# Kernel optimization log

Measured on AMD Instinct MI355X. Metric: run time of the kernel, lower is better.

The kernel has to match this reference:

```python
import jax, jax.numpy as jnp
import numpy as np

N_DIM = 256
N_HEAD = 8
HEAD_DIM = N_DIM // N_HEAD  # 32


def setup_inputs() -> dict:
    key = jax.random.key(0)
    k_x, k_wqkv, k_bqkv, k_wp, k_bp = jax.random.split(key, 5)
    B, T, C = 32, 512, N_DIM
    x = jax.random.normal(k_x, (B, T, C), dtype=jnp.float32)
    # nn.Linear default init ~ U(-1/sqrt(fan_in), 1/sqrt(fan_in)); use scaled normal for simplicity
    s = 1.0 / np.sqrt(C)
    W_qkv = jax.random.normal(k_wqkv, (C, 3 * C), dtype=jnp.float32) * s
    b_qkv = jax.random.normal(k_bqkv, (3 * C,), dtype=jnp.float32) * s
    W_proj = jax.random.normal(k_wp, (C, C), dtype=jnp.float32) * s
    b_proj = jax.random.normal(k_bp, (C,), dtype=jnp.float32) * s
    return {"x": x, "W_qkv": W_qkv, "b_qkv": b_qkv, "W_proj": W_proj, "b_proj": b_proj}


def reference(x, W_qkv, b_qkv, W_proj, b_proj):
    B, T, C = x.shape
    H, D = N_HEAD, HEAD_DIM
    qkv = jnp.einsum('btc,cf->btf', x, W_qkv) + b_qkv  # [B,T,3C]
    q, k, v = jnp.split(qkv, 3, axis=2)
    # [B,T,C] -> [B,H,T,D]
    q = q.reshape(B, T, H, D).transpose(0, 2, 1, 3)
    k = k.reshape(B, T, H, D).transpose(0, 2, 1, 3)
    v = v.reshape(B, T, H, D).transpose(0, 2, 1, 3)
    scale = 1.0 / jnp.sqrt(jnp.float32(D))
    scores = jnp.einsum('bhqd,bhkd->bhqk', q, k) * scale  # [B,H,T,T]
    causal = jnp.tril(jnp.ones((T, T), dtype=bool))
    scores = jnp.where(causal, scores, jnp.finfo(scores.dtype).min)
    attn = jax.nn.softmax(scores, axis=-1)
    out = jnp.einsum('bhqk,bhkd->bhqd', attn, v)  # [B,H,T,D]
    out = out.transpose(0, 2, 1, 3).reshape(B, T, C)
    return jnp.einsum('btc,cf->btf', out, W_proj) + b_proj
```

## Files before the change

kernel.cpp:

```cpp
#include <hip/hip_runtime.h>
#include <stdint.h>
#include <stddef.h>

#define NB 32
#define NT 512
#define NC 256
#define NH 8
#define ND 32
#define NQTOT (NB*NH*NT*ND)

typedef __attribute__((ext_vector_type(8))) short short8;
typedef __attribute__((ext_vector_type(4))) float f32x4;

__device__ __forceinline__ unsigned short f2bf(float f) {
    union { float f; unsigned u; } x; x.f = f;
    unsigned r = (x.u + 0x7FFFu + ((x.u >> 16) & 1u)) >> 16;
    return (unsigned short)r;
}

__global__ __launch_bounds__(256) void k_cvt_w2(const float* __restrict__ wqkv,
                                                unsigned short* __restrict__ wqkvT,
                                                const float* __restrict__ wproj,
                                                unsigned short* __restrict__ wprojT) {
    __shared__ float tile[32][33];
    int bid = blockIdx.x;
    const float* w; unsigned short* wt; int N, bx, by;
    if (bid < 192) { w = wqkv; wt = wqkvT; N = 768; bx = bid % 24; by = bid / 24; }
    else { bid -= 192; w = wproj; wt = wprojT; N = 256; bx = bid % 8; by = bid / 8; }
    const int K = 256;
    const int tx = threadIdx.x & 31;
    const int ty = threadIdx.x >> 5;
    const int n0 = bx * 32, k0 = by * 32;
#pragma unroll
    for (int dy = 0; dy < 4; ++dy)
        tile[ty + dy * 8][tx] = w[(size_t)(k0 + ty + dy * 8) * N + n0 + tx];
    __syncthreads();
#pragma unroll
    for (int dy = 0; dy < 4; ++dy)
        wt[(size_t)(n0 + ty + dy * 8) * K + k0 + tx] = f2bf(tile[tx][ty + dy * 8]);
}

template <int EPI>
__global__ __launch_bounds__(256) void k_gemm(const void* __restrict__ Av,
                                              const unsigned short* __restrict__ Bt,
                                              const float* __restrict__ bias,
                                              unsigned short* __restrict__ qkv,
                                              float* __restrict__ outf,
                                              int M, int N, int K) {
    __shared__ unsigned short Al[2][128][40];
    __shared__ unsigned short Bl[2][128][40];

    const int tid = threadIdx.x;
    const int lane = tid & 63;
    const int w = tid >> 6;
    const int wm = w >> 1, wn = w & 1;
    const int i16 = lane & 15, g = lane >> 4;

    const int nbm = M >> 7;
    const int bm = blockIdx.x % nbm;
    const int bn = blockIdx.x / nbm;
    const int m0 = bm << 7, n0 = bn << 7;

    const float* Af = (const float*)Av;
    const unsigned short* Ab = (const unsigned short*)Av;

    f32x4 acc[4][4];
    const f32x4 z4 = {0.f, 0.f, 0.f, 0.f};
#pragma unroll
    for (int a = 0; a < 4; a++)
#pragma unroll
        for (int b = 0; b < 4; b++) acc[a][b] = z4;

    const int row0 = tid >> 2;
    const int cr = tid & 3;

    float4 fa[2][2];
    short8 sa[2];
    short8 sb[2];

    auto LOAD = [&](int k0) {
#pragma unroll
        for (int h = 0; h < 2; ++h) {
            const int row = row0 + h * 64;
            if (EPI == 0) {
                const float* p = &Af[(size_t)(m0 + row) * K + k0 + cr * 8];
                fa[h][0] = *reinterpret_cast<const float4*>(p);
                fa[h][1] = *reinterpret_cast<const float4*>(p + 4);
            } else {
                sa[h] = *reinterpret_cast<const short8*>(&Ab[(size_t)(m0 + row) * K + k0 + cr * 8]);
            }
            sb[h] = *reinterpret_cast<const short8*>(&Bt[(size_t)(n0 + row) * K + k0 + cr * 8]);
        }
    };
    auto STORE = [&](int buf) {
#pragma unroll
        for (int h = 0; h < 2; ++h) {
            const int row = row0 + h * 64;
            if (EPI == 0) {
                short8 t;
                t[0] = (short)f2bf(fa[h][0].x); t[1] = (short)f2bf(fa[h][0].y);
                t[2] = (short)f2bf(fa[h][0].z); t[3] = (short)f2bf(fa[h][0].w);
                t[4] = (short)f2bf(fa[h][1].x); t[5] = (short)f2bf(fa[h][1].y);
                t[6] = (short)f2bf(fa[h][1].z); t[7] = (short)f2bf(fa[h][1].w);
                *reinterpret_cast<short8*>(&Al[buf][row][cr * 8]) = t;
            } else {
                *reinterpret_cast<short8*>(&Al[buf][row][cr * 8]) = sa[h];
            }
            *reinterpret_cast<short8*>(&Bl[buf][row][cr * 8]) = sb[h];
        }
    };

    LOAD(0);
    STORE(0);
    __syncthreads();

    const int nk = K >> 5;
    for (int it = 0; it < nk; ++it) {
        const int cur = it & 1;
        if (it + 1 < nk) LOAD((it + 1) << 5);

        short8 af[4], bf[4];
#pragma unroll
        for (int mi = 0; mi < 4; mi++)
            af[mi] = *reinterpret_cast<const short8*>(&Al[cur][wm * 64 + mi * 16 + i16][g * 8]);
#pragma unroll
        for (int ni = 0; ni < 4; ni++)
            bf[ni] = *reinterpret_cast<const short8*>(&Bl[cur][wn * 64 + ni * 16 + i16][g * 8]);
#pragma unroll
        for (int mi = 0; mi < 4; mi++)
#pragma unroll
            for (int ni = 0; ni < 4; ni++)
                acc[mi][ni] = __builtin_amdgcn_mfma_f32_16x16x32_bf16(af[mi], bf[ni], acc[mi][ni], 0, 0, 0);

        if (it + 1 < nk) STORE(cur ^ 1);
        __syncthreads();
    }

#pragma unroll
    for (int mi = 0; mi < 4; mi++) {
#pragma unroll
        for (int ni = 0; ni < 4; ni++) {
            const int col = n0 + wn * 64 + ni * 16 + i16;
            const float bv = bias[col];
#pragma unroll
            for (int r = 0; r < 4; r++) {
                const int rowg = m0 + wm * 64 + mi * 16 + g * 4 + r;
                const float v = acc[mi][ni][r] + bv;
                if (EPI == 0) {
                    const int which = col >> 8;
                    const int cc = col & 255;
                    const int h = cc >> 5, d = cc & 31;
                    const int bb = rowg >> 9, t = rowg & 511;
                    qkv[(size_t)which * NQTOT +
                        ((((size_t)bb * NH + h) * NT + t) * ND) + d] = f2bf(v);
                } else {
                    outf[(size_t)rowg * N + col] = v;
                }
            }
        }
    }
}

__global__ __launch_bounds__(256) void k_attn(const unsigned short* __restrict__ qkv,
                                              unsigned short* __restrict__ Ob) {
    __shared__ unsigned short Vt[32][512];
    __shared__ unsigned short Pl[4][16][72];

    const int tid = threadIdx.x;
    const int lane = tid & 63;
    const int w = tid >> 6;
    const int i16 = lane & 15, g = lane >> 4;

    const int half = blockIdx.x >> 8;
    const int bh = blockIdx.x & 255;
    const unsigned short* Qp = qkv + (size_t)bh * NT * ND;
    const unsigned short* Kp = qkv + (size_t)NQTOT + (size_t)bh * NT * ND;
    const unsigned short* Vp = qkv + (size_t)2 * NQTOT + (size_t)bh * NT * ND;

    const int qbase = half * 256 + w * 64;
    const int ktmax = half * 4 + w;
    const int npass = (half + 1) * 4;

    const int srow = tid >> 2;
    const int scr = tid & 3;

    for (int p = 0; p < npass; ++p) {
        short8 v = *reinterpret_cast<const short8*>(&Vp[(p * 64 + srow) * ND + scr * 8]);
#pragma unroll
        for (int j = 0; j < 8; j++) {
            const int swz = j ^ (scr << 1);
            Vt[scr * 8 + j][p * 64 + (srow & 7) + 8 * ((srow >> 3) ^ swz)] = (unsigned short)v[j];
        }
    }

    short8 qf[4];
#pragma unroll
    for (int s = 0; s < 4; s++)
        qf[s] = *reinterpret_cast<const short8*>(&Qp[(qbase + s * 16 + i16) * ND + g * 8]);

    short8 ones;
#pragma unroll
    for (int j = 0; j < 8; j++) ones[j] = (short)0x3F80;

    const f32x4 z4 = {0.f, 0.f, 0.f, 0.f};
    f32x4 O[4][2];
    f32x4 L[4];
#pragma unroll
    for (int s = 0; s < 4; s++) { O[s][0] = z4; O[s][1] = z4; L[s] = z4; }

    __syncthreads();

    const float scale2 = 0.17677669529663687f * 1.4426950408889634f;

    for (int kt = 0; kt <= ktmax; ++kt) {
        short8 kr[4];
#pragma unroll
        for (int kc = 0; kc < 4; kc++)
            kr[kc] = *reinterpret_cast<const short8*>(&Kp[(kt * 64 + kc * 16 + i16) * ND + g * 8]);
        short8 vf[2][2];
#pragma unroll
        for (int kc2 = 0; kc2 < 2; kc2++)
#pragma unroll
            for (int dh = 0; dh < 2; dh++) {
                const int dd = dh * 16 + i16;
                const int swzd = (dd & 7) ^ (((dd >> 3) & 3) << 1);
                vf[kc2][dh] = *reinterpret_cast<const short8*>(
                    &Vt[dd][kt * 64 + 8 * ((kc2 * 4 + g) ^ swzd)]);
            }

        const bool diag = (kt == ktmax);
#pragma unroll
        for (int sub = 0; sub < 4; ++sub) {
            float s[4][4];
#pragma unroll
            for (int kc = 0; kc < 4; kc++) {
                if (!diag || kc <= sub) {
                    f32x4 sv = __builtin_amdgcn_mfma_f32_16x16x32_bf16(kr[kc], qf[sub], z4, 0, 0, 0);
                    if (diag && kc == sub) {
#pragma unroll
                        for (int r = 0; r < 4; r++)
                            s[kc][r] = (g * 4 + r <= i16) ? sv[r] * scale2 : -3e38f;
                    } else {
#pragma unroll
                        for (int r = 0; r < 4; r++) s[kc][r] = sv[r] * scale2;
                    }
                } else {
#pragma unroll
                    for (int r = 0; r < 4; r++) s[kc][r] = -3e38f;
                }
            }

#pragma unroll
            for (int kc = 0; kc < 4; kc++) {
                ushort4 pk;
                pk.x = f2bf(exp2f(s[kc][0])); pk.y = f2bf(exp2f(s[kc][1]));
                pk.z = f2bf(exp2f(s[kc][2])); pk.w = f2bf(exp2f(s[kc][3]));
                *reinterpret_cast<ushort4*>(&Pl[w][i16][kc * 16 + g * 4]) = pk;
            }
            asm volatile("s_waitcnt lgkmcnt(0)" ::: "memory");
            __builtin_amdgcn_sched_barrier(0);

#pragma unroll
            for (int kc2 = 0; kc2 < 2; kc2++) {
                short8 pf = *reinterpret_cast<const short8*>(&Pl[w][i16][kc2 * 32 + g * 8]);
                O[sub][0] = __builtin_amdgcn_mfma_f32_16x16x32_bf16(vf[kc2][0], pf, O[sub][0], 0, 0, 0);
                O[sub][1] = __builtin_amdgcn_mfma_f32_16x16x32_bf16(vf[kc2][1], pf, O[sub][1], 0, 0, 0);
                L[sub]    = __builtin_amdgcn_mfma_f32_16x16x32_bf16(ones,      pf, L[sub],    0, 0, 0);
            }
        }
    }

    const int b = bh >> 3, h = bh & 7;
#pragma unroll
    for (int sub = 0; sub < 4; ++sub) {
        const float inv = 1.f / L[sub][0];
        const int q = qbase + sub * 16 + i16;
        const size_t base = ((size_t)(b * NT + q)) * NC + h * 32;
        ushort4 o0, o1;
        o0.x = f2bf(O[sub][0][0] * inv); o0.y = f2bf(O[sub][0][1] * inv);
        o0.z = f2bf(O[sub][0][2] * inv); o0.w = f2bf(O[sub][0][3] * inv);
        o1.x = f2bf(O[sub][1][0] * inv); o1.y = f2bf(O[sub][1][1] * inv);
        o1.z = f2bf(O[sub][1][2] * inv); o1.w = f2bf(O[sub][1][3] * inv);
        *reinterpret_cast<ushort4*>(&Ob[base + g * 4]) = o0;
        *reinterpret_cast<ushort4*>(&Ob[base + 16 + g * 4]) = o1;
    }
}

extern "C" void kernel_launch(void* const* d_in, const int* in_sizes, int n_in,
                              void* d_out, int out_size, void* d_ws, size_t ws_size,
                              hipStream_t stream) {
    const float* x     = (const float*)d_in[0];
    const float* Wqkv  = (const float*)d_in[1];
    const float* bqkv  = (const float*)d_in[2];
    const float* Wproj = (const float*)d_in[3];
    const float* bproj = (const float*)d_in[4];
    float* out = (float*)d_out;

    unsigned short* WqkvT  = (unsigned short*)d_ws;
    unsigned short* WprojT = WqkvT + (size_t)768 * 256;
    unsigned short* QKV    = WprojT + (size_t)256 * 256;
    unsigned short* Ob     = QKV + (size_t)3 * NQTOT;

    k_cvt_w2<<<256, 256, 0, stream>>>(Wqkv, WqkvT, Wproj, WprojT);

    k_gemm<0><<<128 * 6, 256, 0, stream>>>(x, WqkvT, bqkv, QKV, nullptr, 16384, 768, 256);
    k_attn<<<512, 256, 0, stream>>>(QKV, Ob);
    k_gemm<1><<<128 * 2, 256, 0, stream>>>(Ob, WprojT, bproj, nullptr, out, 16384, 256, 256);
}
```

Before: 124.2 us.

## Balance causal attention work across blocks and prefetch K/V tiles

Reassigns query tiles to the four waves of each attention block so that each block's total causal work is balanced (tile pairs summing to 7) instead of one half doing far more than the other. It also software-pipelines the K tile loads and the V staging loads one step ahead, and raises wave priority around the MFMA section. The aim is less tail imbalance and hidden global-load latency, in exchange for more registers held for the prefetched tiles.

```diff
diff --git a/kernel.cpp b/kernel.cpp
--- a/kernel.cpp
+++ b/kernel.cpp
@@ -171,36 +171,45 @@
     const int w = tid >> 6;
     const int i16 = lane & 15, g = lane >> 4;
 
-    const int half = blockIdx.x >> 8;
+    const int j = blockIdx.x >> 8;
     const int bh = blockIdx.x & 255;
     const unsigned short* Qp = qkv + (size_t)bh * NT * ND;
     const unsigned short* Kp = qkv + (size_t)NQTOT + (size_t)bh * NT * ND;
     const unsigned short* Vp = qkv + (size_t)2 * NQTOT + (size_t)bh * NT * ND;
 
-    const int qbase = half * 256 + w * 64;
-    const int ktmax = half * 4 + w;
-    const int npass = (half + 1) * 4;
+    int c;
+    if (j == 0) c = (w == 0) ? 7 : (w == 1) ? 4 : (w == 2) ? 1 : 2;
+    else        c = (w == 0) ? 0 : (w == 1) ? 3 : (w == 2) ? 6 : 5;
+    const int qbase = c * 64;
+    const int ktmax = c;
+    const int npass = (j == 0) ? 8 : 7;
 
     const int srow = tid >> 2;
     const int scr = tid & 3;
 
-    for (int p = 0; p < npass; ++p) {
-        short8 v = *reinterpret_cast<const short8*>(&Vp[(p * 64 + srow) * ND + scr * 8]);
-#pragma unroll
-        for (int j = 0; j < 8; j++) {
-            const int swz = j ^ (scr << 1);
-            Vt[scr * 8 + j][p * 64 + (srow & 7) + 8 * ((srow >> 3) ^ swz)] = (unsigned short)v[j];
-        }
-    }
-
     short8 qf[4];
 #pragma unroll
     for (int s = 0; s < 4; s++)
         qf[s] = *reinterpret_cast<const short8*>(&Qp[(qbase + s * 16 + i16) * ND + g * 8]);
 
+    {
+        short8 vcur = *reinterpret_cast<const short8*>(&Vp[srow * ND + scr * 8]);
+        for (int p = 0; p < npass; ++p) {
+            short8 vnxt;
+            if (p + 1 < npass)
+                vnxt = *reinterpret_cast<const short8*>(&Vp[((p + 1) * 64 + srow) * ND + scr * 8]);
+#pragma unroll
+            for (int jj = 0; jj < 8; jj++) {
+                const int swz = jj ^ (scr << 1);
+                Vt[scr * 8 + jj][p * 64 + (srow & 7) + 8 * ((srow >> 3) ^ swz)] = (unsigned short)vcur[jj];
+            }
+            vcur = vnxt;
+        }
+    }
+
     short8 ones;
 #pragma unroll
-    for (int j = 0; j < 8; j++) ones[j] = (short)0x3F80;
+    for (int jj = 0; jj < 8; jj++) ones[jj] = (short)0x3F80;
 
     const f32x4 z4 = {0.f, 0.f, 0.f, 0.f};
     f32x4 O[4][2];
@@ -212,11 +221,19 @@
 
     const float scale2 = 0.17677669529663687f * 1.4426950408889634f;
 
+    short8 kr[4], kn[4];
+#pragma unroll
+    for (int kc = 0; kc < 4; kc++)
+        kr[kc] = *reinterpret_cast<const short8*>(&Kp[(kc * 16 + i16) * ND + g * 8]);
+
     for (int kt = 0; kt <= ktmax; ++kt) {
-        short8 kr[4];
-#pragma unroll
-        for (int kc = 0; kc < 4; kc++)
-            kr[kc] = *reinterpret_cast<const short8*>(&Kp[(kt * 64 + kc * 16 + i16) * ND + g * 8]);
+        const bool haveNext = (kt < ktmax);
+        if (haveNext) {
+#pragma unroll
+            for (int kc = 0; kc < 4; kc++)
+                kn[kc] = *reinterpret_cast<const short8*>(
+                    &Kp[((kt + 1) * 64 + kc * 16 + i16) * ND + g * 8]);
+        }
         short8 vf[2][2];
 #pragma unroll
         for (int kc2 = 0; kc2 < 2; kc2++)
@@ -260,6 +277,7 @@
             asm volatile("s_waitcnt lgkmcnt(0)" ::: "memory");
             __builtin_amdgcn_sched_barrier(0);
 
+            __builtin_amdgcn_s_setprio(1);
 #pragma unroll
             for (int kc2 = 0; kc2 < 2; kc2++) {
                 short8 pf = *reinterpret_cast<const short8*>(&Pl[w][i16][kc2 * 32 + g * 8]);
@@ -267,6 +285,11 @@
                 O[sub][1] = __builtin_amdgcn_mfma_f32_16x16x32_bf16(vf[kc2][1], pf, O[sub][1], 0, 0, 0);
                 L[sub]    = __builtin_amdgcn_mfma_f32_16x16x32_bf16(ones,      pf, L[sub],    0, 0, 0);
             }
+            __builtin_amdgcn_s_setprio(0);
+        }
+        if (haveNext) {
+#pragma unroll
+            for (int kc = 0; kc < 4; kc++) kr[kc] = kn[kc];
         }
     }
 
```

New measurement: 126.9 us. 2.2% more time.
